# Performance work log

Hardware: AMD Instinct MI355X
Metric: run time of the kernel (lower is better)

The kernel has to match this reference:

```python
import jax, jax.numpy as jnp
import numpy as np

N_NODES = 100000
N_EDGES = 1600000
D_IN = 64
D_LAT = 64
D_EDGE = 32
N_ACT = 64
NEG_SLOPE = 0.2


def _leaky(x):
    return jnp.where(x > 0, x, NEG_SLOPE * x)


def _gatv2(x, src, dst, eattr, W, b, We, att, bias, n_nodes):
    # GATv2Conv, heads=1, share_weights=True (lin_l == lin_r)
    xl = x @ W + b                                  # [N, out]
    # per-edge message: x_j + x_i + lin_edge(e)
    m = _leaky(xl[src] + xl[dst] + eattr @ We)      # [E, out]
    logits = m @ att                                # [E]
    # segment softmax over destination nodes
    mx = jax.ops.segment_max(logits, dst, num_segments=n_nodes)
    e = jnp.exp(logits - mx[dst])
    denom = jax.ops.segment_sum(e, dst, num_segments=n_nodes)
    alpha = e / denom[dst]                          # [E]
    out = jax.ops.segment_sum(xl[src] * alpha[:, None], dst, num_segments=n_nodes)
    return out + bias


def setup_inputs() -> dict:
    key = jax.random.key(0)
    ks = jax.random.split(key, 13)
    s = 0.05
    x = jax.random.normal(ks[0], (N_NODES, D_IN), dtype=jnp.float32)
    edge_index = jax.random.randint(ks[1], (2, N_EDGES), 0, N_NODES, dtype=jnp.int32)
    edge_attr = jax.random.normal(ks[2], (N_EDGES, D_EDGE), dtype=jnp.float32)
    return {
        "x": x,
        "edge_index": edge_index,
        "edge_attr": edge_attr,
        "W1": jax.random.normal(ks[3], (D_IN, D_LAT), dtype=jnp.float32) * s,
        "b1": jax.random.normal(ks[4], (D_LAT,), dtype=jnp.float32) * s,
        "We1": jax.random.normal(ks[5], (D_EDGE, D_LAT), dtype=jnp.float32) * s,
        "att1": jax.random.normal(ks[6], (D_LAT,), dtype=jnp.float32) * s,
        "bias1": jax.random.normal(ks[7], (D_LAT,), dtype=jnp.float32) * s,
        "W2": jax.random.normal(ks[8], (D_LAT, N_ACT), dtype=jnp.float32) * s,
        "b2": jax.random.normal(ks[9], (N_ACT,), dtype=jnp.float32) * s,
        "We2": jax.random.normal(ks[10], (D_EDGE, N_ACT), dtype=jnp.float32) * s,
        "att2": jax.random.normal(ks[11], (N_ACT,), dtype=jnp.float32) * s,
        "bias2": jax.random.normal(ks[12], (N_ACT,), dtype=jnp.float32) * s,
    }


def reference(x, edge_index, edge_attr, W1, b1, We1, att1, bias1, W2, b2, We2, att2, bias2):
    n = x.shape[0]
    src, dst = edge_index[0], edge_index[1]
    # PyG add_self_loops with fill_value='mean': self-loop edge_attr is the
    # mean of incoming edge attrs per node (0 for isolated nodes).
    deg = jax.ops.segment_sum(jnp.ones_like(dst, dtype=edge_attr.dtype), dst, num_segments=n)
    loop_attr = jax.ops.segment_sum(edge_attr, dst, num_segments=n) / jnp.maximum(deg, 1.0)[:, None]
    ar = jnp.arange(n, dtype=src.dtype)
    src_a = jnp.concatenate([src, ar])
    dst_a = jnp.concatenate([dst, ar])
    ea_a = jnp.concatenate([edge_attr, loop_attr], axis=0)
    h = _gatv2(x, src_a, dst_a, ea_a, W1, b1, We1, att1, bias1, n)
    action_logits = _gatv2(h, src_a, dst_a, ea_a, W2, b2, We2, att2, bias2, n)
    return action_logits
```

## Files before the change

kernel.cpp:

```cpp
#include <hip/hip_runtime.h>
#include <math.h>

#define NN 100000
#define NE 1600000
#define D 64
#define DE 32
#define NB_SCAN ((NN + 255) / 256)

typedef __attribute__((ext_vector_type(8))) short short8;
typedef __attribute__((ext_vector_type(4))) float f32x4;

__device__ __forceinline__ int rfl(int v){ return __builtin_amdgcn_readfirstlane(v); }

#define LEAKY(v) fmaxf((v), 0.2f*(v))

__device__ __forceinline__ unsigned short f2bf(float x){
  unsigned u = __float_as_uint(x);
  unsigned r = (u + 0x7fffu + ((u >> 16) & 1u)) >> 16;
  return (unsigned short)r;
}
__device__ __forceinline__ float bf2f(unsigned short b){
  return __uint_as_float(((unsigned)b) << 16);
}

__global__ __launch_bounds__(256) void k_deg(const int* __restrict__ dst, int* __restrict__ cursor,
                                             int* __restrict__ rank){
  int i = blockIdx.x*256 + threadIdx.x;
  if (i < NE) rank[i] = atomicAdd(&cursor[dst[i]], 1);
}

__global__ __launch_bounds__(256) void k_scan_a(const int* __restrict__ deg, int* __restrict__ bsum){
  __shared__ int sh[256];
  int tid = threadIdx.x;
  int i = blockIdx.x*256 + tid;
  sh[tid] = (i < NN) ? deg[i] : 0;
  __syncthreads();
  for (int s = 128; s > 0; s >>= 1){
    if (tid < s) sh[tid] += sh[tid+s];
    __syncthreads();
  }
  if (tid == 0) bsum[blockIdx.x] = sh[0];
}

__global__ __launch_bounds__(512) void k_scan_b(int* __restrict__ bsum, int* __restrict__ rowptr){
  __shared__ int tmp[512];
  int tid = threadIdx.x;
  int v = (tid < NB_SCAN) ? bsum[tid] : 0;
  tmp[tid] = v;
  __syncthreads();
  for (int off = 1; off < 512; off <<= 1){
    int t = (tid >= off) ? tmp[tid-off] : 0;
    __syncthreads();
    tmp[tid] += t;
    __syncthreads();
  }
  if (tid < NB_SCAN) bsum[tid] = tmp[tid] - v;
  if (tid == 511) rowptr[NN] = tmp[511];
}

__global__ __launch_bounds__(256) void k_scan_c(const int* bsum, int* rowptr, const int* cursor){
  __shared__ int tmp[256];
  int tid = threadIdx.x;
  int i = blockIdx.x*256 + tid;
  int v = (i < NN) ? cursor[i] : 0;
  tmp[tid] = v;
  __syncthreads();
  for (int off = 1; off < 256; off <<= 1){
    int t = (tid >= off) ? tmp[tid-off] : 0;
    __syncthreads();
    tmp[tid] += t;
    __syncthreads();
  }
  if (i < NN){
    rowptr[i] = tmp[tid] - v + bsum[blockIdx.x];
  }
}

__global__ __launch_bounds__(256) void k_scatter(const int* __restrict__ srcp, const int* __restrict__ dstp,
                                                 const int* __restrict__ rank, const int* __restrict__ rowptr,
                                                 const float4* __restrict__ eattr4,
                                                 int* __restrict__ ssrc,
                                                 unsigned short* __restrict__ ea_csr){
  __shared__ int spos[256];
  int tid = threadIdx.x;
  int i = blockIdx.x*256 + tid;
  int pos = 0;
  if (i < NE){
    int d = dstp[i];
    pos = rowptr[d] + rank[i];
    ssrc[pos] = srcp[i];
  }
  spos[tid] = pos;
  __syncthreads();
  int chunk = tid & 7;
  int rbase = blockIdx.x*256;
  #pragma unroll
  for (int k = 0; k < 8; ++k){
    int rl = (tid >> 3) + 32*k;
    int r = rbase + rl;
    if (r < NE){
      float4 v = eattr4[(size_t)r*8 + chunk];
      ushort4 o;
      o.x = f2bf(v.x); o.y = f2bf(v.y); o.z = f2bf(v.z); o.w = f2bf(v.w);
      *(ushort4*)(ea_csr + (size_t)spos[rl]*DE + chunk*4) = o;
    }
  }
}

__global__ __launch_bounds__(256) void k_lin(const float* __restrict__ xin, const float* __restrict__ W,
                                             const float* __restrict__ b, unsigned short* __restrict__ xl){
  int lane = threadIdx.x & 63;
  int q = lane & 15, g = lane >> 4;
  int wid = blockIdx.x*(blockDim.x>>6) + (threadIdx.x>>6);
  int nw = gridDim.x*(blockDim.x>>6);
  short8 wb[2][4];
  #pragma unroll
  for (int kk = 0; kk < 2; ++kk)
    #pragma unroll
    for (int j = 0; j < 4; ++j)
      #pragma unroll
      for (int i = 0; i < 8; ++i)
        wb[kk][j][i] = (short)f2bf(W[(32*kk + 8*g + i)*D + 4*q + j]);
  float4 b4 = *(const float4*)(b + 4*q);
  for (int t0 = wid; t0 < NN/16; t0 += nw){
    int n0 = rfl(t0)*16;
    const float* xr = xin + (size_t)(n0 + q)*D + 8*g;
    float4 a0 = *(const float4*)(xr);
    float4 a1 = *(const float4*)(xr + 4);
    float4 a2 = *(const float4*)(xr + 32);
    float4 a3 = *(const float4*)(xr + 36);
    short8 af0, af1;
    af0[0]=(short)f2bf(a0.x); af0[1]=(short)f2bf(a0.y); af0[2]=(short)f2bf(a0.z); af0[3]=(short)f2bf(a0.w);
    af0[4]=(short)f2bf(a1.x); af0[5]=(short)f2bf(a1.y); af0[6]=(short)f2bf(a1.z); af0[7]=(short)f2bf(a1.w);
    af1[0]=(short)f2bf(a2.x); af1[1]=(short)f2bf(a2.y); af1[2]=(short)f2bf(a2.z); af1[3]=(short)f2bf(a2.w);
    af1[4]=(short)f2bf(a3.x); af1[5]=(short)f2bf(a3.y); af1[6]=(short)f2bf(a3.z); af1[7]=(short)f2bf(a3.w);
    f32x4 acc0 = {b4.x, b4.x, b4.x, b4.x};
    f32x4 acc1 = {b4.y, b4.y, b4.y, b4.y};
    f32x4 acc2 = {b4.z, b4.z, b4.z, b4.z};
    f32x4 acc3 = {b4.w, b4.w, b4.w, b4.w};
    acc0 = __builtin_amdgcn_mfma_f32_16x16x32_bf16(af0, wb[0][0], acc0, 0, 0, 0);
    acc1 = __builtin_amdgcn_mfma_f32_16x16x32_bf16(af0, wb[0][1], acc1, 0, 0, 0);
    acc2 = __builtin_amdgcn_mfma_f32_16x16x32_bf16(af0, wb[0][2], acc2, 0, 0, 0);
    acc3 = __builtin_amdgcn_mfma_f32_16x16x32_bf16(af0, wb[0][3], acc3, 0, 0, 0);
    acc0 = __builtin_amdgcn_mfma_f32_16x16x32_bf16(af1, wb[1][0], acc0, 0, 0, 0);
    acc1 = __builtin_amdgcn_mfma_f32_16x16x32_bf16(af1, wb[1][1], acc1, 0, 0, 0);
    acc2 = __builtin_amdgcn_mfma_f32_16x16x32_bf16(af1, wb[1][2], acc2, 0, 0, 0);
    acc3 = __builtin_amdgcn_mfma_f32_16x16x32_bf16(af1, wb[1][3], acc3, 0, 0, 0);
    #pragma unroll
    for (int i = 0; i < 4; ++i){
      ushort4 pk;
      pk.x = f2bf(acc0[i]); pk.y = f2bf(acc1[i]); pk.z = f2bf(acc2[i]); pk.w = f2bf(acc3[i]);
      *(ushort4*)(xl + (size_t)(n0 + 4*g + i)*D + 4*q) = pk;
    }
  }
}

__global__ __launch_bounds__(256) void k_node(const int* __restrict__ rowptr,
                                              const int* __restrict__ ssrc,
                                              const unsigned short* __restrict__ ea_csr,
                                              const float* __restrict__ We,
                                              const float* __restrict__ att,
                                              const unsigned short* __restrict__ xl,
                                              const float* __restrict__ bias,
                                              float* __restrict__ outp){
  int lane = threadIdx.x & 63;
  int q = lane & 15, g = lane >> 4;
  int wid = blockIdx.x*(blockDim.x>>6) + (threadIdx.x>>6);
  int n0 = wid*4;
  if (n0 >= NN) return;
  short8 wb[4];
  #pragma unroll
  for (int j = 0; j < 4; ++j)
    #pragma unroll
    for (int i = 0; i < 8; ++i)
      wb[j][i] = (short)f2bf(We[(8*g + i)*D + 4*q + j]);
  float4 att4 = *(const float4*)(att + 4*q);
  float4 bi4  = *(const float4*)(bias + 4*q);
  int st_g = rowptr[n0 + g], en_g = rowptr[n0 + g + 1];
  int anode = q >> 2, aoff = q & 3;
  int st_a = rowptr[n0 + anode], en_a = rowptr[n0 + anode + 1];
  int deg = en_g - st_g;
  int dmax = max(deg, __shfl_xor(deg, 16, 64));
  dmax = max(dmax, __shfl_xor(dmax, 32, 64));
  int ntile = (dmax + 3) >> 2;
  ushort4 xdu = *(const ushort4*)(xl + (size_t)(n0 + g)*D + 4*q);
  float xd0 = bf2f(xdu.x), xd1 = bf2f(xdu.y), xd2 = bf2f(xdu.z), xd3 = bf2f(xdu.w);
  float den = 0.f;
  float ac0=0.f, ac1=0.f, ac2=0.f, ac3=0.f;
  float ts0=0.f, ts1=0.f, ts2=0.f, ts3=0.f;

#define LOAD_A(T, DST) { int apos_ = st_a + (T)*4 + aoff; \
  int arow_ = (apos_ < en_a) ? apos_ : ((en_a > st_a) ? (en_a - 1) : 0); \
  DST = *(const short8*)(ea_csr + (size_t)arow_*DE + 8*g); }
#define LOAD_S(T, S0,S1,S2,S3) { int b_ = st_g + (T)*4; \
  S0 = ssrc[(b_   < en_g) ? b_   : 0]; S1 = ssrc[(b_+1 < en_g) ? b_+1 : 0]; \
  S2 = ssrc[(b_+2 < en_g) ? b_+2 : 0]; S3 = ssrc[(b_+3 < en_g) ? b_+3 : 0]; }
#define LOAD_X(S0,S1,S2,S3, X0,X1,X2,X3) { \
  X0 = *(const ushort4*)(xl + (size_t)S0*D + 4*q); \
  X1 = *(const ushort4*)(xl + (size_t)S1*D + 4*q); \
  X2 = *(const ushort4*)(xl + (size_t)S2*D + 4*q); \
  X3 = *(const ushort4*)(xl + (size_t)S3*D + 4*q); }

  short8 aC = {0,0,0,0,0,0,0,0};
  int s0C=0, s1C=0, s2C=0, s3C=0;
  ushort4 x0C={0,0,0,0}, x1C={0,0,0,0}, x2C={0,0,0,0}, x3C={0,0,0,0};
  if (ntile > 0){
    LOAD_A(0, aC);
    LOAD_S(0, s0C, s1C, s2C, s3C);
    LOAD_X(s0C, s1C, s2C, s3C, x0C, x1C, x2C, x3C);
  }
  for (int t = 0; t < ntile; ++t){
    short8 aN = aC;
    int s0N=s0C, s1N=s1C, s2N=s2C, s3N=s3C;
    ushort4 x0N=x0C, x1N=x1C, x2N=x2C, x3N=x3C;
    if (t + 1 < ntile){
      LOAD_A(t+1, aN);
      LOAD_S(t+1, s0N, s1N, s2N, s3N);
      LOAD_X(s0N, s1N, s2N, s3N, x0N, x1N, x2N, x3N);
    }
    __builtin_amdgcn_s_setprio(1);
    f32x4 d0={0.f,0.f,0.f,0.f}, d1={0.f,0.f,0.f,0.f}, d2={0.f,0.f,0.f,0.f}, d3={0.f,0.f,0.f,0.f};
    d0 = __builtin_amdgcn_mfma_f32_16x16x32_bf16(aC, wb[0], d0, 0, 0, 0);
    d1 = __builtin_amdgcn_mfma_f32_16x16x32_bf16(aC, wb[1], d1, 0, 0, 0);
    d2 = __builtin_amdgcn_mfma_f32_16x16x32_bf16(aC, wb[2], d2, 0, 0, 0);
    d3 = __builtin_amdgcn_mfma_f32_16x16x32_bf16(aC, wb[3], d3, 0, 0, 0);
    __builtin_amdgcn_s_setprio(0);
    #pragma unroll
    for (int i = 0; i < 4; ++i){
      int e = st_g + t*4 + i;
      bool valid = (e < en_g);
      ushort4 xu = (i==0) ? x0C : (i==1) ? x1C : (i==2) ? x2C : x3C;
      float x0=bf2f(xu.x), x1=bf2f(xu.y), x2=bf2f(xu.z), x3=bf2f(xu.w);
      float t0 = d0[i], t1 = d1[i], t2 = d2[i], t3 = d3[i];
      float part = att4.x*LEAKY(x0+xd0+t0);
      part = fmaf(att4.y, LEAKY(x1+xd1+t1), part);
      part = fmaf(att4.z, LEAKY(x2+xd2+t2), part);
      part = fmaf(att4.w, LEAKY(x3+xd3+t3), part);
      part += __shfl_xor(part, 1, 64);
      part += __shfl_xor(part, 2, 64);
      part += __shfl_xor(part, 4, 64);
      part += __shfl_xor(part, 8, 64);
      float c = valid ? part : -1e30f;
      float p = __expf(c);
      den += p;
      if (valid){ ts0 += t0; ts1 += t1; ts2 += t2; ts3 += t3; }
      ac0 = fmaf(p, x0, ac0); ac1 = fmaf(p, x1, ac1);
      ac2 = fmaf(p, x2, ac2); ac3 = fmaf(p, x3, ac3);
    }
    aC = aN;
    s0C=s0N; s1C=s1N; s2C=s2N; s3C=s3N;
    x0C=x0N; x1C=x1N; x2C=x2N; x3C=x3N;
  }
  float inv = 1.f / fmaxf((float)deg, 1.f);
  float s0 = fmaf(ts0, inv, xd0 + xd0);
  float s1 = fmaf(ts1, inv, xd1 + xd1);
  float s2 = fmaf(ts2, inv, xd2 + xd2);
  float s3 = fmaf(ts3, inv, xd3 + xd3);
  float cs = att4.x*LEAKY(s0);
  cs = fmaf(att4.y, LEAKY(s1), cs);
  cs = fmaf(att4.z, LEAKY(s2), cs);
  cs = fmaf(att4.w, LEAKY(s3), cs);
  cs += __shfl_xor(cs, 1, 64);
  cs += __shfl_xor(cs, 2, 64);
  cs += __shfl_xor(cs, 4, 64);
  cs += __shfl_xor(cs, 8, 64);
  float ps = __expf(cs);
  den += ps;
  ac0 = fmaf(ps, xd0, ac0); ac1 = fmaf(ps, xd1, ac1);
  ac2 = fmaf(ps, xd2, ac2); ac3 = fmaf(ps, xd3, ac3);
  float4 o;
  float dinv = 1.f / den;
  o.x = fmaf(ac0, dinv, bi4.x);
  o.y = fmaf(ac1, dinv, bi4.y);
  o.z = fmaf(ac2, dinv, bi4.z);
  o.w = fmaf(ac3, dinv, bi4.w);
  *(float4*)(outp + (size_t)(n0 + g)*D + 4*q) = o;
}

extern "C" void kernel_launch(void* const* d_in, const int* in_sizes, int n_in,
                              void* d_out, int out_size, void* d_ws, size_t ws_size,
                              hipStream_t stream){
  const float* x     = (const float*)d_in[0];
  const int*   ei    = (const int*)d_in[1];
  const float* eattr = (const float*)d_in[2];
  const float* W1    = (const float*)d_in[3];
  const float* b1    = (const float*)d_in[4];
  const float* We1   = (const float*)d_in[5];
  const float* att1  = (const float*)d_in[6];
  const float* bias1 = (const float*)d_in[7];
  const float* W2    = (const float*)d_in[8];
  const float* b2    = (const float*)d_in[9];
  const float* We2   = (const float*)d_in[10];
  const float* att2  = (const float*)d_in[11];
  const float* bias2 = (const float*)d_in[12];
  const int* srcp = ei;
  const int* dstp = ei + NE;
  float* out = (float*)d_out;

  char* p = (char*)d_ws;
  size_t off = 0;
  auto alloc = [&](size_t bytes)->char*{
    char* r = p + off; off = (off + bytes + 255) & ~(size_t)255; return r;
  };
  int* rowptr   = (int*)alloc((size_t)(NN+1)*4);
  int* cursor   = (int*)alloc((size_t)NN*4);
  int* bsum     = (int*)alloc(512*4);
  int* rank     = (int*)alloc((size_t)NE*4);
  int* ssrc     = (int*)alloc((size_t)NE*4);
  unsigned short* xl = (unsigned short*)alloc((size_t)NN*D*2);
  float* h      = (float*)alloc((size_t)NN*D*4);
  unsigned short* ea_csr = (unsigned short*)alloc((size_t)NE*DE*2);

  hipMemsetAsync(cursor, 0, (size_t)NN*4, stream);
  k_deg     <<<(NE+255)/256, 256, 0, stream>>>(dstp, cursor, rank);
  k_scan_a  <<<NB_SCAN, 256, 0, stream>>>(cursor, bsum);
  k_scan_b  <<<1, 512, 0, stream>>>(bsum, rowptr);
  k_scan_c  <<<NB_SCAN, 256, 0, stream>>>(bsum, rowptr, cursor);
  k_scatter <<<NE/256, 256, 0, stream>>>(srcp, dstp, rank, rowptr, (const float4*)eattr, ssrc, ea_csr);

  k_lin <<<1600, 256, 0, stream>>>(x, W1, b1, xl);
  k_node<<<6250, 256, 0, stream>>>(rowptr, ssrc, ea_csr, We1, att1, xl, bias1, h);
  k_lin <<<1600, 256, 0, stream>>>(h, W2, b2, xl);
  k_node<<<6250, 256, 0, stream>>>(rowptr, ssrc, ea_csr, We2, att2, xl, bias2, out);
}
```

Measured before the change: 339.4 us.

## Sort destination nodes by degree so each wave processes similar-degree nodes

Adds a degree histogram, a bin scan and a counting sort that permute nodes by in-degree. The CSR is then built in sorted order, and the node kernel looks up the real node id through the permutation. The goal is to cut load imbalance inside a wave, since each wave loops to the max degree of its 4 nodes. In exchange it adds three small kernels, and the destination-node reads and output writes become scattered.

```diff
diff --git a/kernel.cpp b/kernel.cpp
--- a/kernel.cpp
+++ b/kernel.cpp
@@ -29,6 +29,42 @@
   if (i < NE) rank[i] = atomicAdd(&cursor[dst[i]], 1);
 }
 
+__global__ __launch_bounds__(256) void k_hist(const int* __restrict__ deg, int* __restrict__ hist){
+  int n = blockIdx.x*256 + threadIdx.x;
+  if (n < NN) atomicAdd(&hist[min(deg[n], 255)], 1);
+}
+
+__global__ __launch_bounds__(256) void k_binscan(const int* __restrict__ hist,
+                                                 int* __restrict__ binoff, int* __restrict__ bincur){
+  __shared__ int tmp[256];
+  int tid = threadIdx.x;
+  int v = hist[tid];
+  tmp[tid] = v;
+  __syncthreads();
+  for (int off = 1; off < 256; off <<= 1){
+    int t = (tid >= off) ? tmp[tid-off] : 0;
+    __syncthreads();
+    tmp[tid] += t;
+    __syncthreads();
+  }
+  int excl = tmp[tid] - v;
+  binoff[tid] = excl;
+  bincur[tid] = excl;
+}
+
+__global__ __launch_bounds__(256) void k_sort(const int* __restrict__ deg, int* __restrict__ bincur,
+                                              int* __restrict__ perm, int* __restrict__ nrank,
+                                              int* __restrict__ degs){
+  int n = blockIdx.x*256 + threadIdx.x;
+  if (n < NN){
+    int d = deg[n];
+    int sp = atomicAdd(&bincur[min(d, 255)], 1);
+    perm[sp] = n;
+    nrank[n] = sp;
+    degs[sp] = d;
+  }
+}
+
 __global__ __launch_bounds__(256) void k_scan_a(const int* __restrict__ deg, int* __restrict__ bsum){
   __shared__ int sh[256];
   int tid = threadIdx.x;
@@ -58,11 +94,11 @@
   if (tid == 511) rowptr[NN] = tmp[511];
 }
 
-__global__ __launch_bounds__(256) void k_scan_c(const int* bsum, int* rowptr, const int* cursor){
+__global__ __launch_bounds__(256) void k_scan_c(const int* bsum, int* rowptr, const int* degs){
   __shared__ int tmp[256];
   int tid = threadIdx.x;
   int i = blockIdx.x*256 + tid;
-  int v = (i < NN) ? cursor[i] : 0;
+  int v = (i < NN) ? degs[i] : 0;
   tmp[tid] = v;
   __syncthreads();
   for (int off = 1; off < 256; off <<= 1){
@@ -77,7 +113,8 @@
 }
 
 __global__ __launch_bounds__(256) void k_scatter(const int* __restrict__ srcp, const int* __restrict__ dstp,
-                                                 const int* __restrict__ rank, const int* __restrict__ rowptr,
+                                                 const int* __restrict__ rank, const int* __restrict__ nrank,
+                                                 const int* __restrict__ rowptr,
                                                  const float4* __restrict__ eattr4,
                                                  int* __restrict__ ssrc,
                                                  unsigned short* __restrict__ ea_csr){
@@ -87,7 +124,7 @@
   int pos = 0;
   if (i < NE){
     int d = dstp[i];
-    pos = rowptr[d] + rank[i];
+    pos = rowptr[nrank[d]] + rank[i];
     ssrc[pos] = srcp[i];
   }
   spos[tid] = pos;
@@ -156,6 +193,7 @@
 }
 
 __global__ __launch_bounds__(256) void k_node(const int* __restrict__ rowptr,
+                                              const int* __restrict__ perm,
                                               const int* __restrict__ ssrc,
                                               const unsigned short* __restrict__ ea_csr,
                                               const float* __restrict__ We,
@@ -176,6 +214,7 @@
       wb[j][i] = (short)f2bf(We[(8*g + i)*D + 4*q + j]);
   float4 att4 = *(const float4*)(att + 4*q);
   float4 bi4  = *(const float4*)(bias + 4*q);
+  int node_g = perm[n0 + g];
   int st_g = rowptr[n0 + g], en_g = rowptr[n0 + g + 1];
   int anode = q >> 2, aoff = q & 3;
   int st_a = rowptr[n0 + anode], en_a = rowptr[n0 + anode + 1];
@@ -183,7 +222,7 @@
   int dmax = max(deg, __shfl_xor(deg, 16, 64));
   dmax = max(dmax, __shfl_xor(dmax, 32, 64));
   int ntile = (dmax + 3) >> 2;
-  ushort4 xdu = *(const ushort4*)(xl + (size_t)(n0 + g)*D + 4*q);
+  ushort4 xdu = *(const ushort4*)(xl + (size_t)node_g*D + 4*q);
   float xd0 = bf2f(xdu.x), xd1 = bf2f(xdu.y), xd2 = bf2f(xdu.z), xd3 = bf2f(xdu.w);
   float den = 0.f;
   float ac0=0.f, ac1=0.f, ac2=0.f, ac3=0.f;
@@ -274,7 +313,7 @@
   o.y = fmaf(ac1, dinv, bi4.y);
   o.z = fmaf(ac2, dinv, bi4.z);
   o.w = fmaf(ac3, dinv, bi4.w);
-  *(float4*)(outp + (size_t)(n0 + g)*D + 4*q) = o;
+  *(float4*)(outp + (size_t)node_g*D + 4*q) = o;
 }
 
 extern "C" void kernel_launch(void* const* d_in, const int* in_sizes, int n_in,
@@ -302,24 +341,33 @@
   auto alloc = [&](size_t bytes)->char*{
     char* r = p + off; off = (off + bytes + 255) & ~(size_t)255; return r;
   };
+  int* cursor   = (int*)alloc((size_t)(NN+512)*4);
+  int* hist     = cursor + NN;
+  int* bincur   = cursor + NN + 256;
+  int* binoff   = (int*)alloc(256*4);
   int* rowptr   = (int*)alloc((size_t)(NN+1)*4);
-  int* cursor   = (int*)alloc((size_t)NN*4);
   int* bsum     = (int*)alloc(512*4);
   int* rank     = (int*)alloc((size_t)NE*4);
+  int* perm     = (int*)alloc((size_t)NN*4);
+  int* nrank    = (int*)alloc((size_t)NN*4);
+  int* degs     = (int*)alloc((size_t)NN*4);
   int* ssrc     = (int*)alloc((size_t)NE*4);
   unsigned short* xl = (unsigned short*)alloc((size_t)NN*D*2);
   float* h      = (float*)alloc((size_t)NN*D*4);
   unsigned short* ea_csr = (unsigned short*)alloc((size_t)NE*DE*2);
 
-  hipMemsetAsync(cursor, 0, (size_t)NN*4, stream);
+  hipMemsetAsync(cursor, 0, (size_t)(NN+512)*4, stream);
   k_deg     <<<(NE+255)/256, 256, 0, stream>>>(dstp, cursor, rank);
-  k_scan_a  <<<NB_SCAN, 256, 0, stream>>>(cursor, bsum);
+  k_hist    <<<NB_SCAN, 256, 0, stream>>>(cursor, hist);
+  k_binscan <<<1, 256, 0, stream>>>(hist, binoff, bincur);
+  k_sort    <<<NB_SCAN, 256, 0, stream>>>(cursor, bincur, perm, nrank, degs);
+  k_scan_a  <<<NB_SCAN, 256, 0, stream>>>(degs, bsum);
   k_scan_b  <<<1, 512, 0, stream>>>(bsum, rowptr);
-  k_scan_c  <<<NB_SCAN, 256, 0, stream>>>(bsum, rowptr, cursor);
-  k_scatter <<<NE/256, 256, 0, stream>>>(srcp, dstp, rank, rowptr, (const float4*)eattr, ssrc, ea_csr);
+  k_scan_c  <<<NB_SCAN, 256, 0, stream>>>(bsum, rowptr, degs);
+  k_scatter <<<NE/256, 256, 0, stream>>>(srcp, dstp, rank, nrank, rowptr, (const float4*)eattr, ssrc, ea_csr);
 
   k_lin <<<1600, 256, 0, stream>>>(x, W1, b1, xl);
-  k_node<<<6250, 256, 0, stream>>>(rowptr, ssrc, ea_csr, We1, att1, xl, bias1, h);
+  k_node<<<6250, 256, 0, stream>>>(rowptr, perm, ssrc, ea_csr, We1, att1, xl, bias1, h);
   k_lin <<<1600, 256, 0, stream>>>(h, W2, b2, xl);
-  k_node<<<6250, 256, 0, stream>>>(rowptr, ssrc, ea_csr, We2, att2, xl, bias2, out);
-}
+  k_node<<<6250, 256, 0, stream>>>(rowptr, perm, ssrc, ea_csr, We2, att2, xl, bias2, out);
+}
```

After: 859.6 us. 153% more time.
